# Kernel optimization log

Hardware: AMD Instinct MI355X
Metric: run time of the kernel (lower is better)

Reference implementation:

```python
import jax, jax.numpy as jnp
import numpy as np


def squash(s):
    # v = (|s|^2 / (1 + |s|^2)) * s / |s|, norm over last axis
    sn = jnp.sum(s * s, axis=-1, keepdims=True)
    return sn / (1.0 + sn) * s / jnp.sqrt(sn)


def setup_inputs() -> dict:
    key = jax.random.key(0)
    k1, k2, k3 = jax.random.split(key, 3)
    N, C, D, W, H = 32, 32, 16, 16, 16
    K, P = 10, 4
    l = jax.random.normal(k1, (N, C, D, W, H), dtype=jnp.float32)
    g = jax.random.normal(k2, (N, K, D), dtype=jnp.float32)
    weight = jax.random.normal(k3, (1, C, 1, K, P, P), dtype=jnp.float32)
    return {"l": l, "g": g, "weight": weight, "n_rout": 3}


def reference(l, g, weight, n_rout):
    N, C, D, W, H = l.shape
    K = weight.shape[3]
    P = weight.shape[-1]  # D == P*P
    # (N,C,D,W,H) -> (N,C,W*H,P,P)
    lr = jnp.transpose(l, (0, 1, 3, 4, 2)).reshape(N, C, W * H, P, P)
    # per-capsule 4x4 vote matmul against per-(channel,class) weight
    wt = weight[0, :, 0]  # (C,K,P,P)
    V = jnp.einsum('ncsij,ckjd->ncskid', lr, wt)  # (N,C,S,K,P,P)
    B = C * W * H
    V = V.reshape(N, B, K, P * P)  # (N,B,K,D) votes
    # initial logits from global capsule g: b = <g, V> over D
    b = jnp.sum(g[:, None, :, :] * V, axis=-1, keepdims=True)  # (N,B,K,1)
    gc = None
    for _ in range(n_rout):
        c = jax.nn.softmax(b, axis=2)                 # softmax over classes K
        s = jnp.sum(V * c, axis=1, keepdims=True)     # (N,1,K,D)
        gc = squash(s)                                # (N,1,K,D)
        b = jnp.sum(gc * V, axis=-1, keepdims=True)   # (N,B,K,1)
    a = jax.nn.sigmoid(jnp.sqrt(jnp.sum(gc * gc, axis=-1)))  # (N,1,K)
    return a.reshape(N, K), gc.reshape(N, K, P * P)
```

## Files before the change

kernel.cpp:

```cpp
#include <hip/hip_runtime.h>


#define KK 10
#define PP 16
#define CC 32
#define SS 256
#define NN 32

__global__ __launch_bounds__(256, 4) void iter_kernel(
    const float* __restrict__ l,
    const float* __restrict__ w,
    const float* __restrict__ g,
    const float* __restrict__ s_prev,
    float* __restrict__ s_next,
    const int first)
{
  const int bid = blockIdx.x;
  const int n = bid >> 5;
  const int c = bid & 31;
  const int t = threadIdx.x;

  __shared__ float lr_lds[PP][SS + 4];
  __shared__ float ct[KK][SS + 4];
  __shared__ float U_lds[KK * PP];
  __shared__ float w_lds[KK * PP];
  __shared__ float gc_lds[KK * PP];
  __shared__ float f_lds[KK];
  __shared__ float part[KK][PP][PP + 1];

  if (t < KK * PP) w_lds[t] = w[c * KK * PP + t];
  float lr[PP];
  const float* lb = l + (size_t)(n * CC + c) * (PP * SS) + t;
  #pragma unroll
  for (int d = 0; d < PP; ++d) {
    lr[d] = lb[d * SS];
    lr_lds[d][t] = lr[d];
  }

  if (first) {
    if (t < KK * PP) gc_lds[t] = g[n * KK * PP + t];
    __syncthreads();
  } else {
    if (t < KK * PP) gc_lds[t] = s_prev[n * KK * PP + t];
    __syncthreads();
    if (t < KK) {
      float sn = 0.f;
      #pragma unroll
      for (int m = 0; m < PP; ++m) { const float v = gc_lds[t * PP + m]; sn += v * v; }
      f_lds[t] = sn / (1.f + sn) * rsqrtf(sn);
    }
    __syncthreads();
    if (t < KK * PP) gc_lds[t] *= f_lds[t >> 4];
    __syncthreads();
  }

  if (t < KK * PP) {
    const int k = t >> 4, ij = t & 15, i = ij >> 2, j = ij & 3;
    const float4 wv = *(const float4*)&w_lds[k * PP + j * 4];
    const float4 gv = *(const float4*)&gc_lds[k * PP + i * 4];
    U_lds[t] = wv.x * gv.x + wv.y * gv.y + wv.z * gv.z + wv.w * gv.w;
  }
  __syncthreads();

  {
    float b[KK];
    float bmax = -1e30f;
    #pragma unroll
    for (int k = 0; k < KK; ++k) {
      float acc = 0.f;
      #pragma unroll
      for (int d4 = 0; d4 < 4; ++d4) {
        const float4 uv = *(const float4*)&U_lds[k * PP + d4 * 4];
        acc += lr[d4*4+0]*uv.x + lr[d4*4+1]*uv.y + lr[d4*4+2]*uv.z + lr[d4*4+3]*uv.w;
      }
      b[k] = acc;
      bmax = fmaxf(bmax, acc);
    }
    float ssum = 0.f;
    #pragma unroll
    for (int k = 0; k < KK; ++k) { b[k] = __expf(b[k] - bmax); ssum += b[k]; }
    const float inv = 1.f / ssum;
    #pragma unroll
    for (int k = 0; k < KK; ++k) ct[k][t] = b[k] * inv;
  }
  __syncthreads();

  {
    const int ch = t >> 4;
    const int ij = t & 15;
    const int sbase = ch * 16;
    float acc[KK];
    #pragma unroll
    for (int k = 0; k < KK; ++k) acc[k] = 0.f;
    #pragma unroll
    for (int s4 = 0; s4 < 4; ++s4) {
      const float4 lv = *(const float4*)&lr_lds[ij][sbase + s4 * 4];
      #pragma unroll
      for (int k = 0; k < KK; ++k) {
        const float4 cv = *(const float4*)&ct[k][sbase + s4 * 4];
        acc[k] += cv.x*lv.x + cv.y*lv.y + cv.z*lv.z + cv.w*lv.w;
      }
    }
    #pragma unroll
    for (int k = 0; k < KK; ++k) part[k][ij][ch] = acc[k];
  }
  __syncthreads();

  if (t < KK * PP) {
    const int k = t >> 4, ij = t & 15;
    float m = 0.f;
    #pragma unroll
    for (int s4 = 0; s4 < 4; ++s4) {
      const float4 pv = *(const float4*)&part[k][ij][s4 * 4];
      m += pv.x + pv.y + pv.z + pv.w;
    }
    U_lds[t] = m;
  }
  __syncthreads();

  if (t < KK * PP) {
    const int k = t >> 4, i = (t >> 2) & 3, d = t & 3;
    const float* Mp  = U_lds + k * PP + i * 4;
    const float* wpt = w_lds + k * PP + d;
    const float sv = Mp[0]*wpt[0] + Mp[1]*wpt[4] + Mp[2]*wpt[8] + Mp[3]*wpt[12];
    atomicAdd(&s_next[n * KK * PP + t], sv);
  }
}

__global__ __launch_bounds__(256) void final_kernel(
    const float* __restrict__ s_last,
    float* __restrict__ out_a,
    float* __restrict__ out_gc)
{
  const int n = blockIdx.x;
  const int t = threadIdx.x;
  __shared__ float s_lds[KK * PP];
  __shared__ float f_lds[KK];
  if (t < KK * PP) s_lds[t] = s_last[n * KK * PP + t];
  __syncthreads();
  if (t < KK) {
    float sn = 0.f;
    #pragma unroll
    for (int m = 0; m < PP; ++m) { const float v = s_lds[t * PP + m]; sn += v * v; }
    f_lds[t] = sn / (1.f + sn) * rsqrtf(sn);
    const float gn = sn / (1.f + sn);
    out_a[n * KK + t] = 1.f / (1.f + __expf(-gn));
  }
  __syncthreads();
  if (t < KK * PP) out_gc[n * KK * PP + t] = s_lds[t] * f_lds[t >> 4];
}

extern "C" void kernel_launch(void* const* d_in, const int* in_sizes, int n_in,
                              void* d_out, int out_size, void* d_ws, size_t ws_size,
                              hipStream_t stream) {
  const float* l = (const float*)d_in[0];
  const float* g = (const float*)d_in[1];
  const float* w = (const float*)d_in[2];

  float* out    = (float*)d_out;
  float* out_a  = out;
  float* out_gc = out + NN * KK;

  float* s_buf = (float*)d_ws;
  const size_t s_bytes = (size_t)3 * NN * KK * PP * sizeof(float);
  hipMemsetAsync(s_buf, 0, s_bytes, stream);

  float* s0 = s_buf;
  float* s1 = s_buf + NN * KK * PP;
  float* s2 = s_buf + 2 * NN * KK * PP;

  iter_kernel<<<NN * CC, 256, 0, stream>>>(l, w, g, (const float*)nullptr, s0, 1);
  iter_kernel<<<NN * CC, 256, 0, stream>>>(l, w, g, s0, s1, 0);
  iter_kernel<<<NN * CC, 256, 0, stream>>>(l, w, g, s1, s2, 0);
  final_kernel<<<NN, 256, 0, stream>>>(s2, out_a, out_gc);
}
```

Before: 89.46 us.

## Replace memset and final kernel with per-channel partials and last-block finalize

Instead of atomically accumulating into a memset-zeroed buffer, each block writes its per-channel partial sum, and the next iteration reduces the 32 partials when it loads them. The separate memset and final kernel are removed. The last iteration uses atomics plus a per-sample counter, and the block that finishes last for each sample computes the squash and activation outputs. This cuts launch count and the memset, at the cost of a 32-way reduction read in every block and a finalize step that relies on atomics.

```diff
diff --git a/kernel.cpp b/kernel.cpp
--- a/kernel.cpp
+++ b/kernel.cpp
@@ -11,9 +11,13 @@
     const float* __restrict__ l,
     const float* __restrict__ w,
     const float* __restrict__ g,
-    const float* __restrict__ s_prev,
-    float* __restrict__ s_next,
-    const int first)
+    const float* __restrict__ sp_in,
+    float* __restrict__ sp_out,
+    float* __restrict__ s_fin,
+    int* __restrict__ counter,
+    float* __restrict__ out_a,
+    float* __restrict__ out_gc,
+    const int mode)
 {
   const int bid = blockIdx.x;
   const int n = bid >> 5;
@@ -27,6 +31,7 @@
   __shared__ float gc_lds[KK * PP];
   __shared__ float f_lds[KK];
   __shared__ float part[KK][PP][PP + 1];
+  __shared__ int   flag;
 
   if (t < KK * PP) w_lds[t] = w[c * KK * PP + t];
   float lr[PP];
@@ -37,11 +42,21 @@
     lr_lds[d][t] = lr[d];
   }
 
-  if (first) {
+  if (mode == 0) {
     if (t < KK * PP) gc_lds[t] = g[n * KK * PP + t];
     __syncthreads();
   } else {
-    if (t < KK * PP) gc_lds[t] = s_prev[n * KK * PP + t];
+    if (t < KK * PP) {
+      float sv = 0.f;
+      #pragma unroll 8
+      for (int c2 = 0; c2 < CC; ++c2)
+        sv += sp_in[(n * CC + c2) * (KK * PP) + t];
+      gc_lds[t] = sv;
+    }
+    if (mode == 1) {
+      if (c == 1 && t < KK * PP) s_fin[n * KK * PP + t] = 0.f;
+      if (c == 2 && t == 0)      counter[n] = 0;
+    }
     __syncthreads();
     if (t < KK) {
       float sn = 0.f;
@@ -118,36 +133,37 @@
   }
   __syncthreads();
 
+  float sv = 0.f;
   if (t < KK * PP) {
     const int k = t >> 4, i = (t >> 2) & 3, d = t & 3;
     const float* Mp  = U_lds + k * PP + i * 4;
     const float* wpt = w_lds + k * PP + d;
-    const float sv = Mp[0]*wpt[0] + Mp[1]*wpt[4] + Mp[2]*wpt[8] + Mp[3]*wpt[12];
-    atomicAdd(&s_next[n * KK * PP + t], sv);
+    sv = Mp[0]*wpt[0] + Mp[1]*wpt[4] + Mp[2]*wpt[8] + Mp[3]*wpt[12];
   }
-}
 
-__global__ __launch_bounds__(256) void final_kernel(
-    const float* __restrict__ s_last,
-    float* __restrict__ out_a,
-    float* __restrict__ out_gc)
-{
-  const int n = blockIdx.x;
-  const int t = threadIdx.x;
-  __shared__ float s_lds[KK * PP];
-  __shared__ float f_lds[KK];
-  if (t < KK * PP) s_lds[t] = s_last[n * KK * PP + t];
+  if (mode != 2) {
+    if (t < KK * PP) sp_out[(n * CC + c) * (KK * PP) + t] = sv;
+    return;
+  }
+
+  if (t < KK * PP) atomicAdd(&s_fin[n * KK * PP + t], sv);
+  __syncthreads();
+  if (t == 0) flag = (atomicAdd(&counter[n], 1) == CC - 1);
+  __syncthreads();
+  if (!flag) return;
+
+  if (t < KK * PP) U_lds[t] = atomicAdd(&s_fin[n * KK * PP + t], 0.f);
   __syncthreads();
   if (t < KK) {
     float sn = 0.f;
     #pragma unroll
-    for (int m = 0; m < PP; ++m) { const float v = s_lds[t * PP + m]; sn += v * v; }
+    for (int m = 0; m < PP; ++m) { const float v = U_lds[t * PP + m]; sn += v * v; }
     f_lds[t] = sn / (1.f + sn) * rsqrtf(sn);
     const float gn = sn / (1.f + sn);
     out_a[n * KK + t] = 1.f / (1.f + __expf(-gn));
   }
   __syncthreads();
-  if (t < KK * PP) out_gc[n * KK * PP + t] = s_lds[t] * f_lds[t >> 4];
+  if (t < KK * PP) out_gc[n * KK * PP + t] = U_lds[t] * f_lds[t >> 4];
 }
 
 extern "C" void kernel_launch(void* const* d_in, const int* in_sizes, int n_in,
@@ -161,16 +177,15 @@
   float* out_a  = out;
   float* out_gc = out + NN * KK;
 
-  float* s_buf = (float*)d_ws;
-  const size_t s_bytes = (size_t)3 * NN * KK * PP * sizeof(float);
-  hipMemsetAsync(s_buf, 0, s_bytes, stream);
+  float* sp_a    = (float*)d_ws;
+  float* sp_b    = sp_a + NN * CC * KK * PP;
+  float* s_fin   = sp_b + NN * CC * KK * PP;
+  int*   counter = (int*)(s_fin + NN * KK * PP);
 
-  float* s0 = s_buf;
-  float* s1 = s_buf + NN * KK * PP;
-  float* s2 = s_buf + 2 * NN * KK * PP;
-
-  iter_kernel<<<NN * CC, 256, 0, stream>>>(l, w, g, (const float*)nullptr, s0, 1);
-  iter_kernel<<<NN * CC, 256, 0, stream>>>(l, w, g, s0, s1, 0);
-  iter_kernel<<<NN * CC, 256, 0, stream>>>(l, w, g, s1, s2, 0);
-  final_kernel<<<NN, 256, 0, stream>>>(s2, out_a, out_gc);
+  iter_kernel<<<NN * CC, 256, 0, stream>>>(l, w, g, nullptr, sp_a,
+                                           nullptr, nullptr, nullptr, nullptr, 0);
+  iter_kernel<<<NN * CC, 256, 0, stream>>>(l, w, nullptr, sp_a, sp_b,
+                                           s_fin, counter, nullptr, nullptr, 1);
+  iter_kernel<<<NN * CC, 256, 0, stream>>>(l, w, nullptr, sp_b, nullptr,
+                                           s_fin, counter, out_a, out_gc, 2);
 }
```

After: 96.83 us. +8.2%, slower.

## Use bf16 split-precision MFMA for routing logits and weighted sums

Applied to the files above, without the earlier changes.

Replaces the scalar FP32 dot products for the routing logits and the coupling-weighted sum with MFMA 16x16x32 bf16 instructions. Inputs are split into hi/lo bf16 pairs to keep near-FP32 accuracy, and the softmax over classes uses wave shuffles. Atomic accumulation of per-channel partials is replaced by per-block partial stores that the next kernel reduces, which also removes the memset. This adds extra conversion and LDS traffic and lowers occupancy to 2 blocks, and the coupling coefficients are rounded to bf16.

```diff
diff --git a/kernel.cpp b/kernel.cpp
--- a/kernel.cpp
+++ b/kernel.cpp
@@ -7,47 +7,113 @@
 #define SS 256
 #define NN 32
 
-__global__ __launch_bounds__(256, 4) void iter_kernel(
+typedef __attribute__((ext_vector_type(8))) short short8;
+typedef __attribute__((ext_vector_type(4))) float f32x4;
+typedef __attribute__((ext_vector_type(4))) unsigned int uint4v;
+typedef __attribute__((ext_vector_type(2))) unsigned int uint2v;
+
+__device__ inline unsigned short f2bf(float f) {
+  unsigned u = __float_as_uint(f);
+  u += 0x7FFFu + ((u >> 16) & 1u);
+  return (unsigned short)(u >> 16);
+}
+__device__ inline float bf2f(unsigned short h) {
+  return __uint_as_float(((unsigned)h) << 16);
+}
+
+__global__ __launch_bounds__(256, 2) void iter_mfma(
     const float* __restrict__ l,
     const float* __restrict__ w,
     const float* __restrict__ g,
-    const float* __restrict__ s_prev,
-    float* __restrict__ s_next,
-    const int first)
+    const float* __restrict__ sp_in,
+    float* __restrict__ sp_out,
+    const int mode)
 {
-  const int bid = blockIdx.x;
-  const int n = bid >> 5;
-  const int c = bid & 31;
-  const int t = threadIdx.x;
-
-  __shared__ float lr_lds[PP][SS + 4];
-  __shared__ float ct[KK][SS + 4];
-  __shared__ float U_lds[KK * PP];
+  const int bid  = blockIdx.x;
+  const int n    = bid >> 5;
+  const int c    = bid & 31;
+  const int t    = threadIdx.x;
+  const int wv   = t >> 6;
+  const int lrow = t & 15;
+  const int quad = (t >> 4) & 3;
+
+  __shared__ unsigned short lrA_hi[SS * 16];
+  __shared__ unsigned short lrA_lo[SS * 16];
+  __shared__ unsigned short lrB_hi[16 * 264];
+  __shared__ unsigned short lrB_lo[16 * 264];
+  __shared__ unsigned short ct[16 * 264];
+  __shared__ unsigned short U_hi[16 * 24];
+  __shared__ unsigned short U_lo[16 * 24];
+  __shared__ float M_lds[PP * PP];
   __shared__ float w_lds[KK * PP];
   __shared__ float gc_lds[KK * PP];
   __shared__ float f_lds[KK];
-  __shared__ float part[KK][PP][PP + 1];
 
   if (t < KK * PP) w_lds[t] = w[c * KK * PP + t];
-  float lr[PP];
-  const float* lb = l + (size_t)(n * CC + c) * (PP * SS) + t;
-  #pragma unroll
-  for (int d = 0; d < PP; ++d) {
-    lr[d] = lb[d * SS];
-    lr_lds[d][t] = lr[d];
-  }
-
-  if (first) {
+  if (t >= 160 && t < 256) {
+    const int r6 = t - 160;
+    const int kr = 10 + (r6 >> 4), ij = r6 & 15;
+    U_hi[kr * 24 + ij] = 0;
+    U_lo[kr * 24 + ij] = 0;
+  }
+  {
+    float lr[PP];
+    unsigned short hi[PP], lo[PP];
+    const float* lb = l + (size_t)(n * CC + c) * (PP * SS) + t;
+    #pragma unroll
+    for (int d = 0; d < PP; ++d) {
+      lr[d] = lb[d * SS];
+      hi[d] = f2bf(lr[d]);
+      lo[d] = f2bf(lr[d] - bf2f(hi[d]));
+    }
+    uint4v ph0 = { (unsigned)hi[0] | ((unsigned)hi[1] << 16),
+                   (unsigned)hi[2] | ((unsigned)hi[3] << 16),
+                   (unsigned)hi[4] | ((unsigned)hi[5] << 16),
+                   (unsigned)hi[6] | ((unsigned)hi[7] << 16) };
+    uint4v ph1 = { (unsigned)hi[8]  | ((unsigned)hi[9]  << 16),
+                   (unsigned)hi[10] | ((unsigned)hi[11] << 16),
+                   (unsigned)hi[12] | ((unsigned)hi[13] << 16),
+                   (unsigned)hi[14] | ((unsigned)hi[15] << 16) };
+    uint4v pl0 = { (unsigned)lo[0] | ((unsigned)lo[1] << 16),
+                   (unsigned)lo[2] | ((unsigned)lo[3] << 16),
+                   (unsigned)lo[4] | ((unsigned)lo[5] << 16),
+                   (unsigned)lo[6] | ((unsigned)lo[7] << 16) };
+    uint4v pl1 = { (unsigned)lo[8]  | ((unsigned)lo[9]  << 16),
+                   (unsigned)lo[10] | ((unsigned)lo[11] << 16),
+                   (unsigned)lo[12] | ((unsigned)lo[13] << 16),
+                   (unsigned)lo[14] | ((unsigned)lo[15] << 16) };
+    *(uint4v*)&lrA_hi[t * 16]     = ph0;
+    *(uint4v*)&lrA_hi[t * 16 + 8] = ph1;
+    *(uint4v*)&lrA_lo[t * 16]     = pl0;
+    *(uint4v*)&lrA_lo[t * 16 + 8] = pl1;
+    #pragma unroll
+    for (int d = 0; d < PP; ++d) {
+      const int ph = __shfl_xor((int)(unsigned)hi[d], 1);
+      const int pl = __shfl_xor((int)(unsigned)lo[d], 1);
+      if (!(t & 1)) {
+        *(unsigned*)&lrB_hi[d * 264 + t] = (unsigned)hi[d] | (((unsigned)ph) << 16);
+        *(unsigned*)&lrB_lo[d * 264 + t] = (unsigned)lo[d] | (((unsigned)pl) << 16);
+      }
+    }
+  }
+
+  if (mode == 0) {
     if (t < KK * PP) gc_lds[t] = g[n * KK * PP + t];
     __syncthreads();
   } else {
-    if (t < KK * PP) gc_lds[t] = s_prev[n * KK * PP + t];
+    if (t < KK * PP) {
+      float sv = 0.f;
+      #pragma unroll 8
+      for (int c2 = 0; c2 < CC; ++c2)
+        sv += sp_in[(n * CC + c2) * (KK * PP) + t];
+      gc_lds[t] = sv;
+    }
     __syncthreads();
     if (t < KK) {
       float sn = 0.f;
       #pragma unroll
       for (int m = 0; m < PP; ++m) { const float v = gc_lds[t * PP + m]; sn += v * v; }
-      f_lds[t] = sn / (1.f + sn) * rsqrtf(sn);
+      f_lds[t] = (sn > 0.f) ? sn / (1.f + sn) * rsqrtf(sn) : 0.f;
     }
     __syncthreads();
     if (t < KK * PP) gc_lds[t] *= f_lds[t >> 4];
@@ -56,79 +122,94 @@
 
   if (t < KK * PP) {
     const int k = t >> 4, ij = t & 15, i = ij >> 2, j = ij & 3;
-    const float4 wv = *(const float4*)&w_lds[k * PP + j * 4];
-    const float4 gv = *(const float4*)&gc_lds[k * PP + i * 4];
-    U_lds[t] = wv.x * gv.x + wv.y * gv.y + wv.z * gv.z + wv.w * gv.w;
-  }
-  __syncthreads();
-
-  {
-    float b[KK];
-    float bmax = -1e30f;
-    #pragma unroll
-    for (int k = 0; k < KK; ++k) {
-      float acc = 0.f;
+    const float* wp = w_lds + k * PP + j * 4;
+    const float* vp = gc_lds + k * PP + i * 4;
+    const float u = wp[0]*vp[0] + wp[1]*vp[1] + wp[2]*vp[2] + wp[3]*vp[3];
+    const unsigned short uh = f2bf(u);
+    U_hi[k * 24 + ij] = uh;
+    U_lo[k * 24 + ij] = f2bf(u - bf2f(uh));
+  }
+
+  const short8 zs = {0,0,0,0,0,0,0,0};
+  short8 Ahi[4], Alo[4];
+  {
+    const int col8 = (quad & 1) * 8;
+    #pragma unroll
+    for (int tt = 0; tt < 4; ++tt) {
+      const int srow = (wv * 4 + tt) * 16 + lrow;
+      Ahi[tt] = (quad < 2) ? *(const short8*)&lrA_hi[srow * 16 + col8] : zs;
+      Alo[tt] = (quad < 2) ? *(const short8*)&lrA_lo[srow * 16 + col8] : zs;
+    }
+  }
+  __syncthreads();
+
+  {
+    const int col8 = (quad & 1) * 8;
+    const short8 Bhi = (quad < 2) ? *(const short8*)&U_hi[lrow * 24 + col8] : zs;
+    const short8 Blo = (quad < 2) ? *(const short8*)&U_lo[lrow * 24 + col8] : zs;
+    const bool kv = (lrow < KK);
+    #pragma unroll
+    for (int tt = 0; tt < 4; ++tt) {
+      f32x4 a = {0.f, 0.f, 0.f, 0.f};
+      a = __builtin_amdgcn_mfma_f32_16x16x32_bf16(Alo[tt], Bhi, a, 0, 0, 0);
+      a = __builtin_amdgcn_mfma_f32_16x16x32_bf16(Ahi[tt], Blo, a, 0, 0, 0);
+      a = __builtin_amdgcn_mfma_f32_16x16x32_bf16(Ahi[tt], Bhi, a, 0, 0, 0);
+      float cc[4];
       #pragma unroll
-      for (int d4 = 0; d4 < 4; ++d4) {
-        const float4 uv = *(const float4*)&U_lds[k * PP + d4 * 4];
-        acc += lr[d4*4+0]*uv.x + lr[d4*4+1]*uv.y + lr[d4*4+2]*uv.z + lr[d4*4+3]*uv.w;
+      for (int rg = 0; rg < 4; ++rg) {
+        const float bv = a[rg];
+        float mx = kv ? bv : -1e30f;
+        mx = fmaxf(mx, __shfl_xor(mx, 1));
+        mx = fmaxf(mx, __shfl_xor(mx, 2));
+        mx = fmaxf(mx, __shfl_xor(mx, 4));
+        mx = fmaxf(mx, __shfl_xor(mx, 8));
+        float e = kv ? __expf(bv - mx) : 0.f;
+        float sm = e;
+        sm += __shfl_xor(sm, 1);
+        sm += __shfl_xor(sm, 2);
+        sm += __shfl_xor(sm, 4);
+        sm += __shfl_xor(sm, 8);
+        cc[rg] = e / sm;
       }
-      b[k] = acc;
-      bmax = fmaxf(bmax, acc);
-    }
-    float ssum = 0.f;
-    #pragma unroll
-    for (int k = 0; k < KK; ++k) { b[k] = __expf(b[k] - bmax); ssum += b[k]; }
-    const float inv = 1.f / ssum;
-    #pragma unroll
-    for (int k = 0; k < KK; ++k) ct[k][t] = b[k] * inv;
-  }
-  __syncthreads();
-
-  {
-    const int ch = t >> 4;
-    const int ij = t & 15;
-    const int sbase = ch * 16;
-    float acc[KK];
-    #pragma unroll
-    for (int k = 0; k < KK; ++k) acc[k] = 0.f;
-    #pragma unroll
-    for (int s4 = 0; s4 < 4; ++s4) {
-      const float4 lv = *(const float4*)&lr_lds[ij][sbase + s4 * 4];
+      const int scol = (wv * 4 + tt) * 16 + quad * 4;
+      uint2v pk = { (unsigned)f2bf(cc[0]) | (((unsigned)f2bf(cc[1])) << 16),
+                    (unsigned)f2bf(cc[2]) | (((unsigned)f2bf(cc[3])) << 16) };
+      *(uint2v*)&ct[lrow * 264 + scol] = pk;
+    }
+  }
+  __syncthreads();
+
+  {
+    f32x4 mh = {0.f, 0.f, 0.f, 0.f};
+    f32x4 ml = {0.f, 0.f, 0.f, 0.f};
+    #pragma unroll
+    for (int Kt = 0; Kt < 8; ++Kt) {
+      const int off = Kt * 32 + quad * 8;
+      const short8 af = *(const short8*)&ct[lrow * 264 + off];
+      mh = __builtin_amdgcn_mfma_f32_16x16x32_bf16(
+               af, *(const short8*)&lrB_hi[lrow * 264 + off], mh, 0, 0, 0);
+      ml = __builtin_amdgcn_mfma_f32_16x16x32_bf16(
+               af, *(const short8*)&lrB_lo[lrow * 264 + off], ml, 0, 0, 0);
+    }
+    if (t < 64) {
       #pragma unroll
-      for (int k = 0; k < KK; ++k) {
-        const float4 cv = *(const float4*)&ct[k][sbase + s4 * 4];
-        acc[k] += cv.x*lv.x + cv.y*lv.y + cv.z*lv.z + cv.w*lv.w;
-      }
-    }
-    #pragma unroll
-    for (int k = 0; k < KK; ++k) part[k][ij][ch] = acc[k];
-  }
-  __syncthreads();
-
-  if (t < KK * PP) {
-    const int k = t >> 4, ij = t & 15;
-    float m = 0.f;
-    #pragma unroll
-    for (int s4 = 0; s4 < 4; ++s4) {
-      const float4 pv = *(const float4*)&part[k][ij][s4 * 4];
-      m += pv.x + pv.y + pv.z + pv.w;
-    }
-    U_lds[t] = m;
+      for (int rg = 0; rg < 4; ++rg)
+        M_lds[(quad * 4 + rg) * PP + lrow] = mh[rg] + ml[rg];
+    }
   }
   __syncthreads();
 
   if (t < KK * PP) {
     const int k = t >> 4, i = (t >> 2) & 3, d = t & 3;
-    const float* Mp  = U_lds + k * PP + i * 4;
-    const float* wpt = w_lds + k * PP + d;
-    const float sv = Mp[0]*wpt[0] + Mp[1]*wpt[4] + Mp[2]*wpt[8] + Mp[3]*wpt[12];
-    atomicAdd(&s_next[n * KK * PP + t], sv);
+    const float* Mp = M_lds + k * PP + i * 4;
+    const float* wp = w_lds + k * PP + d;
+    sp_out[(n * CC + c) * (KK * PP) + t] =
+        Mp[0]*wp[0] + Mp[1]*wp[4] + Mp[2]*wp[8] + Mp[3]*wp[12];
   }
 }
 
 __global__ __launch_bounds__(256) void final_kernel(
-    const float* __restrict__ s_last,
+    const float* __restrict__ sp_in,
     float* __restrict__ out_a,
     float* __restrict__ out_gc)
 {
@@ -136,13 +217,19 @@
   const int t = threadIdx.x;
   __shared__ float s_lds[KK * PP];
   __shared__ float f_lds[KK];
-  if (t < KK * PP) s_lds[t] = s_last[n * KK * PP + t];
+  if (t < KK * PP) {
+    float sv = 0.f;
+    #pragma unroll 8
+    for (int c2 = 0; c2 < CC; ++c2)
+      sv += sp_in[(n * CC + c2) * (KK * PP) + t];
+    s_lds[t] = sv;
+  }
   __syncthreads();
   if (t < KK) {
     float sn = 0.f;
     #pragma unroll
     for (int m = 0; m < PP; ++m) { const float v = s_lds[t * PP + m]; sn += v * v; }
-    f_lds[t] = sn / (1.f + sn) * rsqrtf(sn);
+    f_lds[t] = (sn > 0.f) ? sn / (1.f + sn) * rsqrtf(sn) : 0.f;
     const float gn = sn / (1.f + sn);
     out_a[n * KK + t] = 1.f / (1.f + __expf(-gn));
   }
@@ -153,6 +240,7 @@
 extern "C" void kernel_launch(void* const* d_in, const int* in_sizes, int n_in,
                               void* d_out, int out_size, void* d_ws, size_t ws_size,
                               hipStream_t stream) {
+  (void)in_sizes; (void)n_in; (void)out_size; (void)ws_size;
   const float* l = (const float*)d_in[0];
   const float* g = (const float*)d_in[1];
   const float* w = (const float*)d_in[2];
@@ -161,16 +249,12 @@
   float* out_a  = out;
   float* out_gc = out + NN * KK;
 
-  float* s_buf = (float*)d_ws;
-  const size_t s_bytes = (size_t)3 * NN * KK * PP * sizeof(float);
-  hipMemsetAsync(s_buf, 0, s_bytes, stream);
-
-  float* s0 = s_buf;
-  float* s1 = s_buf + NN * KK * PP;
-  float* s2 = s_buf + 2 * NN * KK * PP;
-
-  iter_kernel<<<NN * CC, 256, 0, stream>>>(l, w, g, (const float*)nullptr, s0, 1);
-  iter_kernel<<<NN * CC, 256, 0, stream>>>(l, w, g, s0, s1, 0);
-  iter_kernel<<<NN * CC, 256, 0, stream>>>(l, w, g, s1, s2, 0);
-  final_kernel<<<NN, 256, 0, stream>>>(s2, out_a, out_gc);
-}
+  float* sp_a = (float*)d_ws;
+  float* sp_b = sp_a + NN * CC * KK * PP;
+  float* sp_c = sp_b + NN * CC * KK * PP;
+
+  iter_mfma<<<NN * CC, 256, 0, stream>>>(l, w, g, nullptr, sp_a, 0);
+  iter_mfma<<<NN * CC, 256, 0, stream>>>(l, w, nullptr, sp_a, sp_b, 1);
+  iter_mfma<<<NN * CC, 256, 0, stream>>>(l, w, nullptr, sp_b, sp_c, 1);
+  final_kernel<<<NN, 256, 0, stream>>>(sp_c, out_a, out_gc);
+}
```

Result: slower. 115.3 us (+28.9%).
